# Kernel tuning notes

Hardware: AMD Instinct MI355X
Metric: run time of the kernel (lower is better)

Reference implementation:

```python
import jax, jax.numpy as jnp
import numpy as np

GAMMA = 10.0
EPS = 1e-6  # epsilon from __init__
B, D, C = 128, 1024, 1000


def setup_inputs() -> dict:
    key = jax.random.key(0)
    k1, k2, k3, k4 = jax.random.split(key, 4)
    return {
        "activations": jax.random.normal(k1, (B, D), jnp.float32),
        "W": jax.random.normal(k2, (D, C), jnp.float32) * 0.02,
        "b": jax.random.normal(k3, (C,), jnp.float32) * 0.02,
        "targets": jax.random.randint(k4, (B,), 0, C),
    }


def reference(activations, W, b, targets):
    # Linear classifier head: logits must be a differentiable fn of activations
    def head(a):  # [D] -> [C]
        return a @ W + b

    logits = jax.vmap(head)(activations)          # [B, C]
    # Batched Jacobian replaces the per-(i,j) torch.autograd.grad loop.
    J = jax.vmap(jax.jacrev(head))(activations)   # [B, C, D]

    t1h = jax.nn.one_hot(targets, C, dtype=logits.dtype)       # [B, C]
    correct = jnp.sum(logits * t1h, axis=1)                    # [B]
    grad_correct = jnp.einsum('bcd,bc->bd', J, t1h)            # [B, D]

    grad_diff = J - grad_correct[:, None, :]                   # [B, C, D]
    # dual norm (l2): sqrt(sum sq + eps), then forward adds +eps again
    dual_norm = jnp.sqrt(jnp.sum(grad_diff * grad_diff, axis=2) + EPS) + EPS  # [B, C]

    score_diff = logits - correct[:, None]                     # [B, C]
    violation = jax.nn.relu(GAMMA + score_diff / dual_norm)    # [B, C]
    violation = violation * (1.0 - t1h)  # exclude target class (relu >= 0 so max unaffected)

    loss = jnp.max(violation, axis=1)  # aggregation = 'max' over incorrect classes
    return jnp.mean(loss)
```

## Files before the change

kernel.cpp:

```cpp
#include <hip/hip_runtime.h>
#include <math.h>

#define Bn 128
#define Dn 1024
#define Cn 1000
#define Cpad 1024
#define GAMMA 10.0f
#define EPSv 1e-6f

#define DCH 8
#define DSPAN (Dn / DCH)
#define BM 4


__global__ __launch_bounds__(256) void k_pass1(
    const float* __restrict__ A, const float* __restrict__ W,
    const int* __restrict__ tgt,
    float* __restrict__ ws_lg, float* __restrict__ ws_dot,
    float* __restrict__ ws_nrm)
{
    const int tid    = threadIdx.x;
    const int cchunk = blockIdx.x;
    const int bg     = blockIdx.y;
    const int dchunk = blockIdx.z;
    const int b0 = bg * BM;
    const int d0 = dchunk * DSPAN;
    const int c  = cchunk * 512 + tid * 2;
    const bool valid = (c < Cn);
    const int cl = valid ? c : 0;

    __shared__ float4 AsI[DSPAN];
    __shared__ float4 WtI[DSPAN];

    for (int e = tid; e < DSPAN * BM; e += 256) {
        int i = e & (DSPAN - 1);
        int j = e >> 7;
        ((float*)&AsI[i])[j] = A[(b0 + j) * Dn + d0 + i];
        ((float*)&WtI[i])[j] = W[(d0 + i) * Cn + tgt[b0 + j]];
    }
    __syncthreads();

    float lgx[BM] = {0.f, 0.f, 0.f, 0.f}, lgy[BM] = {0.f, 0.f, 0.f, 0.f};
    float dtx[BM] = {0.f, 0.f, 0.f, 0.f}, dty[BM] = {0.f, 0.f, 0.f, 0.f};
    float sqx = 0.f, sqy = 0.f;

    const float* Wp = W + (size_t)d0 * Cn + cl;
    #pragma unroll 8
    for (int i = 0; i < DSPAN; ++i) {
        const float2 w = *(const float2*)(Wp + (size_t)i * Cn);
        const float4 a4 = AsI[i];
        const float4 t4 = WtI[i];
        const float ax[4] = {a4.x, a4.y, a4.z, a4.w};
        const float tx[4] = {t4.x, t4.y, t4.z, t4.w};
        #pragma unroll
        for (int j = 0; j < BM; ++j) {
            lgx[j] = fmaf(ax[j], w.x, lgx[j]);
            lgy[j] = fmaf(ax[j], w.y, lgy[j]);
            dtx[j] = fmaf(tx[j], w.x, dtx[j]);
            dty[j] = fmaf(tx[j], w.y, dty[j]);
        }
        sqx = fmaf(w.x, w.x, sqx);
        sqy = fmaf(w.y, w.y, sqy);
    }

    if (valid) {
        #pragma unroll
        for (int j = 0; j < BM; ++j) {
            atomicAdd(&ws_lg [(b0 + j) * Cpad + c    ], lgx[j]);
            atomicAdd(&ws_lg [(b0 + j) * Cpad + c + 1], lgy[j]);
            atomicAdd(&ws_dot[(b0 + j) * Cpad + c    ], dtx[j]);
            atomicAdd(&ws_dot[(b0 + j) * Cpad + c + 1], dty[j]);
        }
        if (bg == 0) {
            atomicAdd(&ws_nrm[c    ], sqx);
            atomicAdd(&ws_nrm[c + 1], sqy);
        }
    }
}

__global__ __launch_bounds__(256) void k_pass2(
    const float* __restrict__ ws_lg, const float* __restrict__ ws_dot,
    const float* __restrict__ ws_nrm, const float* __restrict__ bias,
    const int* __restrict__ tgt, float* __restrict__ out)
{
    const int b = blockIdx.x;
    const int tid = threadIdx.x;
    const int t = tgt[b];
    const float correct = ws_lg[b * Cpad + t] + bias[t];
    const float nt = ws_nrm[t];

    float m = 0.f;
    for (int c = tid; c < Cn; c += 256) {
        if (c == t) continue;
        float lg   = ws_lg [b * Cpad + c] + bias[c];
        float dist = ws_nrm[c] + nt - 2.f * ws_dot[b * Cpad + c];
        float dn   = sqrtf(dist + EPSv) + EPSv;
        float v    = GAMMA + (lg - correct) / dn;
        m = fmaxf(m, v);
    }
    for (int off = 32; off; off >>= 1) m = fmaxf(m, __shfl_down(m, off, 64));
    __shared__ float sm[4];
    if ((tid & 63) == 0) sm[tid >> 6] = m;
    __syncthreads();
    if (tid == 0) {
        float bm = fmaxf(fmaxf(sm[0], sm[1]), fmaxf(sm[2], sm[3]));
        atomicAdd(out, bm * (1.0f / (float)Bn));
    }
}

extern "C" void kernel_launch(void* const* d_in, const int* in_sizes, int n_in,
                              void* d_out, int out_size, void* d_ws, size_t ws_size,
                              hipStream_t stream) {
    const float* A    = (const float*)d_in[0];
    const float* W    = (const float*)d_in[1];
    const float* bias = (const float*)d_in[2];
    const int*   tgt  = (const int*)d_in[3];
    float* out = (float*)d_out;

    float* ws_lg  = (float*)d_ws;
    float* ws_dot = ws_lg + Bn * Cpad;
    float* ws_nrm = ws_dot + Bn * Cpad;
    const size_t ws_floats = (size_t)2 * Bn * Cpad + Cpad;

    hipMemsetAsync(d_ws, 0, ws_floats * sizeof(float), stream);
    hipMemsetAsync(d_out, 0, sizeof(float), stream);

    k_pass1<<<dim3(2, Bn / BM / 1, DCH), dim3(256), 0, stream>>>(
        A, W, tgt, ws_lg, ws_dot, ws_nrm);
    k_pass2<<<dim3(Bn), dim3(256), 0, stream>>>(ws_lg, ws_dot, ws_nrm, bias, tgt, out);
}
```

Baseline: 99.18 us.

## Replace atomic accumulation with per-chunk partial buffers and drop memsets

The first kernel now writes per-D-chunk partial logits, target dot products and column norms with plain float4 stores into separate slices, and no longer uses atomicAdd into a zeroed workspace. The final kernel sums the 16 partials itself, and the output is zeroed inside the first kernel, so both hipMemsetAsync calls go away. Each thread now covers 4 classes with float4 W loads, and the D split doubles to 16 chunks. This removes the memset launches and atomic contention, but uses a much larger workspace and makes the final kernel read all the partials. It also clamps the distance at zero.

```diff
diff --git a/kernel.cpp b/kernel.cpp
--- a/kernel.cpp
+++ b/kernel.cpp
@@ -8,102 +8,136 @@
 #define GAMMA 10.0f
 #define EPSv 1e-6f
 
-#define DCH 8
+#define DCH 16
 #define DSPAN (Dn / DCH)
 #define BM 4
+#define NBG (Bn / BM)
 
 
-__global__ __launch_bounds__(256) void k_pass1(
+__global__ __launch_bounds__(256) void lm_partial(
     const float* __restrict__ A, const float* __restrict__ W,
     const int* __restrict__ tgt,
-    float* __restrict__ ws_lg, float* __restrict__ ws_dot,
-    float* __restrict__ ws_nrm)
+    float* __restrict__ lg, float* __restrict__ dt,
+    float* __restrict__ nrm, float* __restrict__ out)
 {
-    const int tid    = threadIdx.x;
-    const int cchunk = blockIdx.x;
-    const int bg     = blockIdx.y;
-    const int dchunk = blockIdx.z;
+    const int tid = threadIdx.x;
+    const int bg  = blockIdx.x;
+    const int k   = blockIdx.y;
+    if (bg == 0 && k == 0 && tid == 0) out[0] = 0.f;
+
     const int b0 = bg * BM;
-    const int d0 = dchunk * DSPAN;
-    const int c  = cchunk * 512 + tid * 2;
-    const bool valid = (c < Cn);
-    const int cl = valid ? c : 0;
+    const int d0 = k * DSPAN;
+    const int c0 = tid * 4;
+    const bool valid = (c0 < Cn);
+    const int c0m = valid ? c0 : 0;
 
     __shared__ float4 AsI[DSPAN];
     __shared__ float4 WtI[DSPAN];
-
-    for (int e = tid; e < DSPAN * BM; e += 256) {
-        int i = e & (DSPAN - 1);
-        int j = e >> 7;
+    {
+        const int i = tid & (DSPAN - 1);
+        const int j = tid >> 6;
         ((float*)&AsI[i])[j] = A[(b0 + j) * Dn + d0 + i];
-        ((float*)&WtI[i])[j] = W[(d0 + i) * Cn + tgt[b0 + j]];
+        ((float*)&WtI[i])[j] = W[(size_t)(d0 + i) * Cn + tgt[b0 + j]];
     }
     __syncthreads();
 
-    float lgx[BM] = {0.f, 0.f, 0.f, 0.f}, lgy[BM] = {0.f, 0.f, 0.f, 0.f};
-    float dtx[BM] = {0.f, 0.f, 0.f, 0.f}, dty[BM] = {0.f, 0.f, 0.f, 0.f};
-    float sqx = 0.f, sqy = 0.f;
+    float aL[BM][4], aD[BM][4], aN[4];
+    #pragma unroll
+    for (int e = 0; e < 4; ++e) {
+        aN[e] = 0.f;
+        #pragma unroll
+        for (int j = 0; j < BM; ++j) { aL[j][e] = 0.f; aD[j][e] = 0.f; }
+    }
 
-    const float* Wp = W + (size_t)d0 * Cn + cl;
-    #pragma unroll 8
+    const float* Wp = W + (size_t)d0 * Cn + c0m;
+    #pragma unroll 4
     for (int i = 0; i < DSPAN; ++i) {
-        const float2 w = *(const float2*)(Wp + (size_t)i * Cn);
+        const float4 w  = *(const float4*)(Wp + (size_t)i * Cn);
         const float4 a4 = AsI[i];
         const float4 t4 = WtI[i];
-        const float ax[4] = {a4.x, a4.y, a4.z, a4.w};
-        const float tx[4] = {t4.x, t4.y, t4.z, t4.w};
+        const float wv[4] = {w.x, w.y, w.z, w.w};
+        const float av[4] = {a4.x, a4.y, a4.z, a4.w};
+        const float tv[4] = {t4.x, t4.y, t4.z, t4.w};
         #pragma unroll
-        for (int j = 0; j < BM; ++j) {
-            lgx[j] = fmaf(ax[j], w.x, lgx[j]);
-            lgy[j] = fmaf(ax[j], w.y, lgy[j]);
-            dtx[j] = fmaf(tx[j], w.x, dtx[j]);
-            dty[j] = fmaf(tx[j], w.y, dty[j]);
+        for (int e = 0; e < 4; ++e) {
+            aN[e] = fmaf(wv[e], wv[e], aN[e]);
+            #pragma unroll
+            for (int j = 0; j < BM; ++j) {
+                aL[j][e] = fmaf(av[j], wv[e], aL[j][e]);
+                aD[j][e] = fmaf(tv[j], wv[e], aD[j][e]);
+            }
         }
-        sqx = fmaf(w.x, w.x, sqx);
-        sqy = fmaf(w.y, w.y, sqy);
     }
 
     if (valid) {
         #pragma unroll
         for (int j = 0; j < BM; ++j) {
-            atomicAdd(&ws_lg [(b0 + j) * Cpad + c    ], lgx[j]);
-            atomicAdd(&ws_lg [(b0 + j) * Cpad + c + 1], lgy[j]);
-            atomicAdd(&ws_dot[(b0 + j) * Cpad + c    ], dtx[j]);
-            atomicAdd(&ws_dot[(b0 + j) * Cpad + c + 1], dty[j]);
+            const size_t off = ((size_t)(k * Bn + b0 + j)) * Cpad + c0;
+            *(float4*)&lg[off] = make_float4(aL[j][0], aL[j][1], aL[j][2], aL[j][3]);
+            *(float4*)&dt[off] = make_float4(aD[j][0], aD[j][1], aD[j][2], aD[j][3]);
         }
-        if (bg == 0) {
-            atomicAdd(&ws_nrm[c    ], sqx);
-            atomicAdd(&ws_nrm[c + 1], sqy);
-        }
+        if (bg == 0)
+            *(float4*)&nrm[(size_t)k * Cpad + c0] =
+                make_float4(aN[0], aN[1], aN[2], aN[3]);
     }
 }
 
-__global__ __launch_bounds__(256) void k_pass2(
-    const float* __restrict__ ws_lg, const float* __restrict__ ws_dot,
-    const float* __restrict__ ws_nrm, const float* __restrict__ bias,
+__global__ __launch_bounds__(256) void lm_final(
+    const float* __restrict__ lg, const float* __restrict__ dt,
+    const float* __restrict__ nrm, const float* __restrict__ bias,
     const int* __restrict__ tgt, float* __restrict__ out)
 {
     const int b = blockIdx.x;
     const int tid = threadIdx.x;
     const int t = tgt[b];
-    const float correct = ws_lg[b * Cpad + t] + bias[t];
-    const float nt = ws_nrm[t];
+
+    __shared__ float s_cr, s_nt;
+    if (tid == 0) {
+        float cr = 0.f, nt = 0.f;
+        #pragma unroll
+        for (int k = 0; k < DCH; ++k) {
+            cr += lg[((size_t)(k * Bn + b)) * Cpad + t];
+            nt += nrm[(size_t)k * Cpad + t];
+        }
+        s_cr = cr + bias[t];
+        s_nt = nt;
+    }
+    __syncthreads();
 
     float m = 0.f;
-    for (int c = tid; c < Cn; c += 256) {
-        if (c == t) continue;
-        float lg   = ws_lg [b * Cpad + c] + bias[c];
-        float dist = ws_nrm[c] + nt - 2.f * ws_dot[b * Cpad + c];
-        float dn   = sqrtf(dist + EPSv) + EPSv;
-        float v    = GAMMA + (lg - correct) / dn;
-        m = fmaxf(m, v);
+    if (tid < 250) {
+        const int c0 = tid * 4;
+        float L[4] = {0.f,0.f,0.f,0.f}, Dt[4] = {0.f,0.f,0.f,0.f}, Nr[4] = {0.f,0.f,0.f,0.f};
+        #pragma unroll
+        for (int k = 0; k < DCH; ++k) {
+            const float4 l4 = *(const float4*)&lg[((size_t)(k * Bn + b)) * Cpad + c0];
+            const float4 d4 = *(const float4*)&dt[((size_t)(k * Bn + b)) * Cpad + c0];
+            const float4 n4 = *(const float4*)&nrm[(size_t)k * Cpad + c0];
+            L[0] += l4.x; L[1] += l4.y; L[2] += l4.z; L[3] += l4.w;
+            Dt[0] += d4.x; Dt[1] += d4.y; Dt[2] += d4.z; Dt[3] += d4.w;
+            Nr[0] += n4.x; Nr[1] += n4.y; Nr[2] += n4.z; Nr[3] += n4.w;
+        }
+        const float4 bi = *(const float4*)&bias[c0];
+        const float bv[4] = {bi.x, bi.y, bi.z, bi.w};
+        const float cr = s_cr, nt = s_nt;
+        #pragma unroll
+        for (int e = 0; e < 4; ++e) {
+            const int c = c0 + e;
+            if (c != t) {
+                float dist = fmaxf(Nr[e] + nt - 2.f * Dt[e], 0.f);
+                float dn   = sqrtf(dist + EPSv) + EPSv;
+                float v    = GAMMA + (L[e] + bv[e] - cr) / dn;
+                m = fmaxf(m, v);
+            }
+        }
     }
+
     for (int off = 32; off; off >>= 1) m = fmaxf(m, __shfl_down(m, off, 64));
     __shared__ float sm[4];
     if ((tid & 63) == 0) sm[tid >> 6] = m;
     __syncthreads();
     if (tid == 0) {
-        float bm = fmaxf(fmaxf(sm[0], sm[1]), fmaxf(sm[2], sm[3]));
+        const float bm = fmaxf(fmaxf(sm[0], sm[1]), fmaxf(sm[2], sm[3]));
         atomicAdd(out, bm * (1.0f / (float)Bn));
     }
 }
@@ -117,15 +151,10 @@
     const int*   tgt  = (const int*)d_in[3];
     float* out = (float*)d_out;
 
-    float* ws_lg  = (float*)d_ws;
-    float* ws_dot = ws_lg + Bn * Cpad;
-    float* ws_nrm = ws_dot + Bn * Cpad;
-    const size_t ws_floats = (size_t)2 * Bn * Cpad + Cpad;
+    float* lg  = (float*)d_ws;
+    float* dt  = lg + (size_t)DCH * Bn * Cpad;
+    float* nrm = dt + (size_t)DCH * Bn * Cpad;
 
-    hipMemsetAsync(d_ws, 0, ws_floats * sizeof(float), stream);
-    hipMemsetAsync(d_out, 0, sizeof(float), stream);
-
-    k_pass1<<<dim3(2, Bn / BM / 1, DCH), dim3(256), 0, stream>>>(
-        A, W, tgt, ws_lg, ws_dot, ws_nrm);
-    k_pass2<<<dim3(Bn), dim3(256), 0, stream>>>(ws_lg, ws_dot, ws_nrm, bias, tgt, out);
+    lm_partial<<<dim3(NBG, DCH), dim3(256), 0, stream>>>(A, W, tgt, lg, dt, nrm, out);
+    lm_final<<<dim3(Bn), dim3(256), 0, stream>>>(lg, dt, nrm, bias, tgt, out);
 }
```

Measured after the change: 87.36 us. 11.9% less time.
